# Kernel tuning notes

Measured on AMD Instinct MI355X. Metric: run time of the kernel, lower is better.

Reference implementation:

```python
import jax, jax.numpy as jnp
import numpy as np
from jax import lax

NUM_HEADS = 8
HEAD_DIM = 32  # filters_per_head


def conv1d_same(x, w, b):
    # x: [B, T, Cin], w: [K, Cin, Cout] (WIO), 'same' padding, stride 1
    y = lax.conv_general_dilated(x, w, window_strides=(1,), padding='SAME',
                                 dimension_numbers=('NWC', 'WIO', 'NWC'))
    return y + b


def setup_inputs() -> dict:
    key = jax.random.key(0)
    ks = jax.random.split(key, 9)
    B, T, C = 8, 2048, 256
    K = 3
    s = 1.0 / np.sqrt(K * C)
    return {
        'x': jax.random.normal(ks[0], (B, T, C), dtype=jnp.float32),
        'Wq': jax.random.normal(ks[1], (K, C, C), dtype=jnp.float32) * s,
        'bq': jnp.zeros((C,), dtype=jnp.float32),
        'Wk': jax.random.normal(ks[2], (K, C, C), dtype=jnp.float32) * s,
        'bk': jnp.zeros((C,), dtype=jnp.float32),
        'Wv': jax.random.normal(ks[3], (K, C, C), dtype=jnp.float32) * s,
        'bv': jnp.zeros((C,), dtype=jnp.float32),
        'Wo': jax.random.normal(ks[4], (K, C, C), dtype=jnp.float32) * s,
        'bo': jnp.zeros((C,), dtype=jnp.float32),
    }


def reference(x, Wq, bq, Wk, bk, Wv, bv, Wo, bo):
    B, T, C = x.shape
    q = conv1d_same(x, Wq, bq)
    k = conv1d_same(x, Wk, bk)
    v = conv1d_same(x, Wv, bv)

    def split(t):  # [B, T, C] -> [B, H, T, D]
        return t.reshape(B, T, NUM_HEADS, HEAD_DIM).transpose(0, 2, 1, 3)

    q, k, v = split(q), split(k), split(v)
    scale = 1.0 / jnp.sqrt(jnp.float32(HEAD_DIM))
    logits = jnp.einsum('bhqd,bhkd->bhqk', q, k) * scale  # [B,H,T,T]
    attn = jax.nn.softmax(logits, axis=-1)
    ctx = jnp.einsum('bhqk,bhkd->bhqd', attn, v)
    ctx = ctx.transpose(0, 2, 1, 3).reshape(B, T, C)
    out = x + conv1d_same(ctx, Wo, bo)
    return out
```

## Files before the change

### kernel.cpp

```cpp
#include <hip/hip_runtime.h>
#include <math.h>

#define BDIM 8
#define TDIM 2048
#define CDIM 256
#define HDIM 8
#define DDIM 32
#define TP   (TDIM + 2)

typedef __attribute__((ext_vector_type(8))) short bf16x8;
typedef __attribute__((ext_vector_type(4))) float f32x4;

#if __has_builtin(__builtin_amdgcn_exp2f)
#define EXP2(x) __builtin_amdgcn_exp2f(x)
#else
#define EXP2(x) exp2f(x)
#endif

__device__ __forceinline__ unsigned pk2(float lo, float hi) {
    union { float f; unsigned u; } a, b;
    a.f = lo; b.f = hi;
    return __builtin_amdgcn_perm(b.u + 0x8000u, a.u + 0x8000u, 0x07060302u);
}
__device__ __forceinline__ unsigned pk2t(float lo, float hi) {
    union { float f; unsigned u; } a, b;
    a.f = lo; b.f = hi;
    return __builtin_amdgcn_perm(b.u, a.u, 0x07060302u);
}
__device__ __forceinline__ short bf1(float v) {
    union { float f; unsigned u; } a; a.f = v;
    return (short)((a.u + 0x8000u) >> 16);
}
__device__ __forceinline__ void gld16(const short* g, short* l) {
    __builtin_amdgcn_global_load_lds((const __attribute__((address_space(1))) void*)g,
                                     (__attribute__((address_space(3))) void*)l, 16, 0, 0);
}

#define XBLK 832
#define WBLK 192

__global__ __launch_bounds__(256) void prep_kernel(
    const float* __restrict__ x,
    const float* __restrict__ Wq, const float* __restrict__ Wk,
    const float* __restrict__ Wv, const float* __restrict__ Wo,
    short* __restrict__ xbfp, short* __restrict__ cp,
    short* __restrict__ wcat, short* __restrict__ wot)
{
    const int tid = threadIdx.x;
    if (blockIdx.x < XBLK) {
        const int NX = BDIM * TDIM * 64;
        const int NH = 4096;
        unsigned* xw = (unsigned*)xbfp;
        unsigned* cw = (unsigned*)cp;
        for (int i = blockIdx.x * 256 + tid; i < NX + NH; i += XBLK * 256) {
            if (i < NX) {
                const int bt = i >> 6, c4 = i & 63;
                const int b = bt >> 11, t = bt & 2047;
                const float4 f = *(const float4*)(x + (size_t)bt * 256 + c4 * 4);
                const size_t wo_ = (size_t)(b * TP + t + 1) * 128 + c4 * 2;
                xw[wo_]     = pk2(f.x, f.y);
                xw[wo_ + 1] = pk2(f.z, f.w);
            } else {
                const int hz = i - NX;
                const int half = hz >> 11, z = hz & 2047;
                const int b = z >> 8, r = (z >> 7) & 1, wofs = z & 127;
                const size_t w_ = ((size_t)b * TP + (size_t)r * (TP - 1)) * 128 + wofs;
                if (half == 0) xw[w_] = 0u; else cw[w_] = 0u;
            }
        }
    } else {
        __shared__ float xs[64][65];
        const int wb = blockIdx.x - XBLK;
        const int pair = wb >> 4, sub = wb & 15;
        const int dt = pair >> 2, mat = pair & 3;
        const int ci0 = (sub >> 2) * 64, co0 = (sub & 3) * 64;
        const float* W = mat == 0 ? Wq : mat == 1 ? Wk : mat == 2 ? Wv : Wo;
        const float* src = W + dt * 65536 + (size_t)ci0 * 256 + co0;
        for (int idx = tid; idx < 4096; idx += 256) {
            const int r = idx >> 6, c = idx & 63;
            xs[r][c] = src[(size_t)r * 256 + c];
        }
        __syncthreads();
        short* dstbase = (mat < 3) ? (wcat + (size_t)(mat * 256 + co0) * 768)
                                   : (wot + (size_t)co0 * 768);
        for (int idx = tid; idx < 512; idx += 256) {
            const int co_l = idx >> 3, ci_l = (idx & 7) * 8;
            uint4 u;
            u.x = pk2(xs[ci_l + 0][co_l], xs[ci_l + 1][co_l]);
            u.y = pk2(xs[ci_l + 2][co_l], xs[ci_l + 3][co_l]);
            u.z = pk2(xs[ci_l + 4][co_l], xs[ci_l + 5][co_l]);
            u.w = pk2(xs[ci_l + 6][co_l], xs[ci_l + 7][co_l]);
            *(uint4*)(dstbase + (size_t)co_l * 768 + dt * 256 + ci0 + ci_l) = u;
        }
    }
}

__global__ __launch_bounds__(256) void gemm_qkv(
    const short* __restrict__ xbfp, const short* __restrict__ wcat,
    const float* __restrict__ bq, const float* __restrict__ bk,
    const float* __restrict__ bv,
    short* __restrict__ qo, short* __restrict__ ko, short* __restrict__ vt2)
{
    __shared__ short As[2][4096];
    __shared__ short Bs[2][4096];
    const int tid = threadIdx.x;
    const int wv = tid >> 6, lane = tid & 63, quad = lane >> 4, col = lane & 15;
    const int bx = blockIdx.x;
    const int b = bx >> 4, t0 = (bx & 15) * 128;
    const int by = blockIdx.y;
    const int qkv = by >> 1;
    const int m0 = by * 128;

    const short* wA = wcat + (size_t)m0 * 768;
    const short* xB = xbfp + ((size_t)b * TP + t0) * CDIM;
    const int r0 = tid >> 2, s0 = (tid & 3) * 8;

#define STAGE_Q(kk, bsel) do {                                                  \
    const int dt_ = (kk) >> 3, ci0_ = ((kk) & 7) * 32, k0_ = (kk) * 32;         \
    gld16(wA + (size_t)r0 * 768 + k0_ + s0,        &As[bsel][tid * 8]);         \
    gld16(wA + (size_t)(r0 + 64) * 768 + k0_ + s0, &As[bsel][tid * 8 + 2048]);  \
    gld16(xB + (size_t)(r0 + dt_) * 256 + ci0_ + s0,      &Bs[bsel][tid * 8]);  \
    gld16(xB + (size_t)(r0 + 64 + dt_) * 256 + ci0_ + s0, &Bs[bsel][tid * 8 + 2048]); \
} while (0)

    STAGE_Q(0, 0);

    const float* bias = qkv == 0 ? bq : qkv == 1 ? bk : bv;
    f32x4 acc[4][4];
#pragma unroll
    for (int mt = 0; mt < 4; ++mt) {
        const int cb = ((m0 + (wv & 1) * 64 + mt * 16) & 255) + quad * 4;
        const float4 b4 = *(const float4*)(bias + cb);
#pragma unroll
        for (int nt = 0; nt < 4; ++nt) acc[mt][nt] = (f32x4){b4.x, b4.y, b4.z, b4.w};
    }

    int bsel = 0;
    for (int kk = 0; kk < 24; ++kk) {
        __syncthreads();
        if (kk < 23) STAGE_Q(kk + 1, bsel ^ 1);
        const short* Ab = &As[bsel][((wv & 1) * 64 + col) * 32 + quad * 8];
        const short* Bb = &Bs[bsel][((wv >> 1) * 64 + col) * 32 + quad * 8];
        bf16x8 af[4], bfr[4];
#pragma unroll
        for (int i = 0; i < 4; ++i) {
            af[i]  = *(const bf16x8*)(Ab + i * 512);
            bfr[i] = *(const bf16x8*)(Bb + i * 512);
        }
#pragma unroll
        for (int mt = 0; mt < 4; ++mt)
#pragma unroll
            for (int nt = 0; nt < 4; ++nt)
                acc[mt][nt] = __builtin_amdgcn_mfma_f32_16x16x32_bf16(af[mt], bfr[nt], acc[mt][nt], 0, 0, 0);
        bsel ^= 1;
    }

    const float qs = 0.25503000508221157f;
#pragma unroll
    for (int mt = 0; mt < 4; ++mt) {
        const int cocat = m0 + (wv & 1) * 64 + mt * 16 + quad * 4;
        const int co = cocat & 255;
        const int hh = co >> 5, d = co & 31;
        const size_t bh = (size_t)b * HDIM + hh;
#pragma unroll
        for (int nt = 0; nt < 4; ++nt) {
            const int t = t0 + (wv >> 1) * 64 + nt * 16 + col;
            const f32x4 a = acc[mt][nt];
            if (qkv == 0) {
                uint2 u = make_uint2(pk2(a[0] * qs, a[1] * qs), pk2(a[2] * qs, a[3] * qs));
                *(uint2*)(qo + (bh * TDIM + t) * DDIM + d) = u;
            } else if (qkv == 1) {
                uint2 u = make_uint2(pk2(a[0], a[1]), pk2(a[2], a[3]));
                *(uint2*)(ko + (bh * TDIM + t) * DDIM + d) = u;
            } else {
                const int kt = t >> 6, u6 = t & 63, kg = u6 >> 5, rr = u6 & 31;
                const int j = ((rr >> 4) << 2) | (rr & 3), qd = (rr >> 2) & 3;
                short* vb2 = vt2 + ((bh * 32 + kt) * 2 + kg) * 1024 + qd * 8 + j;
#pragma unroll
                for (int r = 0; r < 4; ++r) vb2[(d + r) * 32] = bf1(a[r]);
            }
        }
    }
#undef STAGE_Q
}

__global__ __launch_bounds__(256) void gemm_res(
    const short* __restrict__ cp, const short* __restrict__ wot,
    const float* __restrict__ bo, const float* __restrict__ x,
    float* __restrict__ out)
{
    __shared__ short As[2][4096];
    __shared__ short Bs[2][4096];
    const int tid = threadIdx.x;
    const int wv = tid >> 6, lane = tid & 63, quad = lane >> 4, col = lane & 15;
    const int bx = blockIdx.x;
    const int b = bx >> 4, t0 = (bx & 15) * 128;
    const int m0 = blockIdx.y * 128;

    const short* wA = wot + (size_t)m0 * 768;
    const short* cB = cp + ((size_t)b * TP + t0) * CDIM;
    const int r0 = tid >> 2, s0 = (tid & 3) * 8;

#define STAGE_R(kk, bsel) do {                                                  \
    const int dt_ = (kk) >> 3, ci0_ = ((kk) & 7) * 32, k0_ = (kk) * 32;         \
    gld16(wA + (size_t)r0 * 768 + k0_ + s0,        &As[bsel][tid * 8]);         \
    gld16(wA + (size_t)(r0 + 64) * 768 + k0_ + s0, &As[bsel][tid * 8 + 2048]);  \
    gld16(cB + (size_t)(r0 + dt_) * 256 + ci0_ + s0,      &Bs[bsel][tid * 8]);  \
    gld16(cB + (size_t)(r0 + 64 + dt_) * 256 + ci0_ + s0, &Bs[bsel][tid * 8 + 2048]); \
} while (0)

    STAGE_R(0, 0);

    f32x4 acc[4][4];
#pragma unroll
    for (int mt = 0; mt < 4; ++mt) {
        const int cb = m0 + (wv & 1) * 64 + mt * 16 + quad * 4;
        const float4 b4 = *(const float4*)(bo + cb);
#pragma unroll
        for (int nt = 0; nt < 4; ++nt) acc[mt][nt] = (f32x4){b4.x, b4.y, b4.z, b4.w};
    }

    int bsel = 0;
    for (int kk = 0; kk < 24; ++kk) {
        __syncthreads();
        if (kk < 23) STAGE_R(kk + 1, bsel ^ 1);
        const short* Ab = &As[bsel][((wv & 1) * 64 + col) * 32 + quad * 8];
        const short* Bb = &Bs[bsel][((wv >> 1) * 64 + col) * 32 + quad * 8];
        bf16x8 af[4], bfr[4];
#pragma unroll
        for (int i = 0; i < 4; ++i) {
            af[i]  = *(const bf16x8*)(Ab + i * 512);
            bfr[i] = *(const bf16x8*)(Bb + i * 512);
        }
#pragma unroll
        for (int mt = 0; mt < 4; ++mt)
#pragma unroll
            for (int nt = 0; nt < 4; ++nt)
                acc[mt][nt] = __builtin_amdgcn_mfma_f32_16x16x32_bf16(af[mt], bfr[nt], acc[mt][nt], 0, 0, 0);
        bsel ^= 1;
    }

#pragma unroll
    for (int mt = 0; mt < 4; ++mt) {
        const int co = m0 + (wv & 1) * 64 + mt * 16 + quad * 4;
#pragma unroll
        for (int nt = 0; nt < 4; ++nt) {
            const int t = t0 + (wv >> 1) * 64 + nt * 16 + col;
            const size_t o = ((size_t)b * TDIM + t) * CDIM + co;
            const float4 xv = *(const float4*)(x + o);
            const f32x4 a = acc[mt][nt];
            *(float4*)(out + o) = make_float4(a[0] + xv.x, a[1] + xv.y, a[2] + xv.z, a[3] + xv.w);
        }
    }
#undef STAGE_R
}

__global__ __launch_bounds__(256, 4) void attn_kernel(
    const short* __restrict__ q, const short* __restrict__ k,
    const short* __restrict__ vt2, short* __restrict__ cp)
{
    const int tid = threadIdx.x;
    const int wv = tid >> 6, lane = tid & 63, quad = lane >> 4, col = lane & 15;
    const int bh = blockIdx.x;
    const int q0 = blockIdx.y * 128 + wv * 32;

    const short* qb = q + (size_t)bh * TDIM * DDIM;
    const int fo = col * 32 + quad * 8;
    const short* kp = k   + (size_t)bh * TDIM * DDIM + fo;
    const short* vp = vt2 + (size_t)bh * TDIM * DDIM + fo;

    bf16x8 qf[2];
    qf[0] = *(const bf16x8*)(qb + (size_t)(q0 + col) * DDIM + quad * 8);
    qf[1] = *(const bf16x8*)(qb + (size_t)(q0 + 16 + col) * DDIM + quad * 8);

    f32x4 acc0[2] = {{0.f,0.f,0.f,0.f},{0.f,0.f,0.f,0.f}};
    f32x4 acc1[2] = {{0.f,0.f,0.f,0.f},{0.f,0.f,0.f,0.f}};
    f32x4 accl[2] = {{0.f,0.f,0.f,0.f},{0.f,0.f,0.f,0.f}};
    const f32x4 zero = {0.f, 0.f, 0.f, 0.f};
    const short one_bf = (short)0x3F80;
    const bf16x8 ones = {one_bf, one_bf, one_bf, one_bf, one_bf, one_bf, one_bf, one_bf};

    bf16x8 kc[4], vf[4];
#pragma unroll
    for (int g = 0; g < 4; ++g) {
        kc[g] = *(const bf16x8*)(kp + g * 512);
        vf[g] = *(const bf16x8*)(vp + g * 512);
    }

#pragma unroll 2
    for (int kt = 0; kt < TDIM / 64; ++kt) {
        const int ntile = (kt + 1) & (TDIM / 64 - 1);
        bf16x8 kn[4], vn[4];
#pragma unroll
        for (int g = 0; g < 4; ++g) {
            kn[g] = *(const bf16x8*)(kp + ntile * 2048 + g * 512);
            vn[g] = *(const bf16x8*)(vp + ntile * 2048 + g * 512);
        }
#pragma unroll
        for (int qi = 0; qi < 2; ++qi) {
            f32x4 s[4];
            __builtin_amdgcn_s_setprio(1);
#pragma unroll
            for (int g = 0; g < 4; ++g)
                s[g] = __builtin_amdgcn_mfma_f32_16x16x32_bf16(kc[g], qf[qi], zero, 0, 0, 0);
            __builtin_amdgcn_s_setprio(0);
            float p[16];
#pragma unroll
            for (int g = 0; g < 4; ++g)
#pragma unroll
                for (int r = 0; r < 4; ++r)
                    p[g * 4 + r] = EXP2(s[g][r]);
            union { unsigned u[4]; bf16x8 v; } P0, P1;
            P0.u[0] = pk2t(p[0], p[1]);   P0.u[1] = pk2t(p[2], p[3]);
            P0.u[2] = pk2t(p[4], p[5]);   P0.u[3] = pk2t(p[6], p[7]);
            P1.u[0] = pk2t(p[8], p[9]);   P1.u[1] = pk2t(p[10], p[11]);
            P1.u[2] = pk2t(p[12], p[13]); P1.u[3] = pk2t(p[14], p[15]);
            __builtin_amdgcn_s_setprio(1);
            acc0[qi] = __builtin_amdgcn_mfma_f32_16x16x32_bf16(vf[0], P0.v, acc0[qi], 0, 0, 0);
            acc1[qi] = __builtin_amdgcn_mfma_f32_16x16x32_bf16(vf[1], P0.v, acc1[qi], 0, 0, 0);
            accl[qi] = __builtin_amdgcn_mfma_f32_16x16x32_bf16(ones,  P0.v, accl[qi], 0, 0, 0);
            acc0[qi] = __builtin_amdgcn_mfma_f32_16x16x32_bf16(vf[2], P1.v, acc0[qi], 0, 0, 0);
            acc1[qi] = __builtin_amdgcn_mfma_f32_16x16x32_bf16(vf[3], P1.v, acc1[qi], 0, 0, 0);
            accl[qi] = __builtin_amdgcn_mfma_f32_16x16x32_bf16(ones,  P1.v, accl[qi], 0, 0, 0);
            __builtin_amdgcn_s_setprio(0);
        }
#pragma unroll
        for (int g = 0; g < 4; ++g) { kc[g] = kn[g]; vf[g] = vn[g]; }
    }

    const int b = bh >> 3, hh = bh & 7;
#pragma unroll
    for (int qi = 0; qi < 2; ++qi) {
        const float inv = 1.f / accl[qi][0];
        const int t = q0 + qi * 16 + col;
        short* crow = cp + ((size_t)b * TP + t + 1) * CDIM + hh * DDIM;
        uint2 u0 = make_uint2(pk2(acc0[qi][0] * inv, acc0[qi][1] * inv),
                              pk2(acc0[qi][2] * inv, acc0[qi][3] * inv));
        uint2 u1 = make_uint2(pk2(acc1[qi][0] * inv, acc1[qi][1] * inv),
                              pk2(acc1[qi][2] * inv, acc1[qi][3] * inv));
        *(uint2*)(crow + quad * 4)      = u0;
        *(uint2*)(crow + 16 + quad * 4) = u1;
    }
}

extern "C" void kernel_launch(void* const* d_in, const int* in_sizes, int n_in,
                              void* d_out, int out_size, void* d_ws, size_t ws_size,
                              hipStream_t stream) {
    const float* x  = (const float*)d_in[0];
    const float* Wq = (const float*)d_in[1];
    const float* bq = (const float*)d_in[2];
    const float* Wk = (const float*)d_in[3];
    const float* bk = (const float*)d_in[4];
    const float* Wv = (const float*)d_in[5];
    const float* bv = (const float*)d_in[6];
    const float* Wo = (const float*)d_in[7];
    const float* bo = (const float*)d_in[8];
    float* out = (float*)d_out;

    short* p = (short*)d_ws;
    short* xbfp = p; p += (size_t)BDIM * TP * CDIM;
    short* cpb  = p; p += (size_t)BDIM * TP * CDIM;
    short* qbuf = p; p += (size_t)BDIM * HDIM * TDIM * DDIM;
    short* kbuf = p; p += (size_t)BDIM * HDIM * TDIM * DDIM;
    short* vt2  = p; p += (size_t)BDIM * HDIM * TDIM * DDIM;
    short* wcat = p; p += 768 * 768;
    short* wot  = p; p += 256 * 768;

    prep_kernel<<<dim3(XBLK + WBLK), 256, 0, stream>>>(x, Wq, Wk, Wv, Wo, xbfp, cpb, wcat, wot);
    gemm_qkv<<<dim3(128, 6), 256, 0, stream>>>(xbfp, wcat, bq, bk, bv, qbuf, kbuf, vt2);
    attn_kernel<<<dim3(64, 16), 256, 0, stream>>>(qbuf, kbuf, vt2, cpb);
    gemm_res<<<dim3(128, 2), 256, 0, stream>>>(cpb, wot, bo, x, out);
}
```

Measured before the change: 202.1 us.

## Stage K/V tiles through double-buffered swizzled LDS in attention kernel

The attention kernel now loads each 128-key K and V tile cooperatively into double-buffered shared memory with async global-to-LDS copies and an XOR swizzle, instead of having every wave read K/V directly from global memory into registers. The four waves of a block share each tile, so redundant global/L2 traffic is cut and the next tile is prefetched while the current one is computed. The key tile per iteration doubles from 64 to 128, which raises register pressure (8 K and 8 V fragments, 32 probabilities) and adds a block-wide barrier per iteration.

```diff
diff --git a/kernel.cpp b/kernel.cpp
--- a/kernel.cpp
+++ b/kernel.cpp
@@ -259,15 +259,32 @@
     const short* __restrict__ q, const short* __restrict__ k,
     const short* __restrict__ vt2, short* __restrict__ cp)
 {
+    __shared__ short ks[2][4096];
+    __shared__ short vs[2][4096];
     const int tid = threadIdx.x;
     const int wv = tid >> 6, lane = tid & 63, quad = lane >> 4, col = lane & 15;
     const int bh = blockIdx.x;
     const int q0 = blockIdx.y * 128 + wv * 32;
 
     const short* qb = q + (size_t)bh * TDIM * DDIM;
-    const int fo = col * 32 + quad * 8;
-    const short* kp = k   + (size_t)bh * TDIM * DDIM + fo;
-    const short* vp = vt2 + (size_t)bh * TDIM * DDIM + fo;
+    const short* kb = k + (size_t)bh * TDIM * DDIM;
+    const short* vb = vt2 + (size_t)bh * TDIM * DDIM;
+
+    const int c1 = tid, c2 = tid + 256;
+    const int g1 = ((c1 & ~3) | ((c1 & 3) ^ ((c1 >> 3) & 3))) * 8;
+    const int g2 = ((c2 & ~3) | ((c2 & 3) ^ ((c2 >> 3) & 3))) * 8;
+    const int l1 = c1 * 8, l2 = c2 * 8;
+
+#define STAGE_A(kt, bsel) do {                                   \
+    const short* kt_k = kb + (kt) * 4096;                        \
+    const short* kt_v = vb + (kt) * 4096;                        \
+    gld16(kt_k + g1, &ks[bsel][l1]);                             \
+    gld16(kt_k + g2, &ks[bsel][l2]);                             \
+    gld16(kt_v + g1, &vs[bsel][l1]);                             \
+    gld16(kt_v + g2, &vs[bsel][l2]);                             \
+} while (0)
+
+    STAGE_A(0, 0);
 
     bf16x8 qf[2];
     qf[0] = *(const bf16x8*)(qb + (size_t)(q0 + col) * DDIM + quad * 8);
@@ -280,52 +297,52 @@
     const short one_bf = (short)0x3F80;
     const bf16x8 ones = {one_bf, one_bf, one_bf, one_bf, one_bf, one_bf, one_bf, one_bf};
 
-    bf16x8 kc[4], vf[4];
-#pragma unroll
-    for (int g = 0; g < 4; ++g) {
-        kc[g] = *(const bf16x8*)(kp + g * 512);
-        vf[g] = *(const bf16x8*)(vp + g * 512);
-    }
-
+    const int foff = col * 32 + ((quad ^ ((col >> 1) & 3)) << 3);
+    __syncthreads();
+
+    int bsel = 0;
 #pragma unroll 2
-    for (int kt = 0; kt < TDIM / 64; ++kt) {
-        const int ntile = (kt + 1) & (TDIM / 64 - 1);
-        bf16x8 kn[4], vn[4];
-#pragma unroll
-        for (int g = 0; g < 4; ++g) {
-            kn[g] = *(const bf16x8*)(kp + ntile * 2048 + g * 512);
-            vn[g] = *(const bf16x8*)(vp + ntile * 2048 + g * 512);
+    for (int kt = 0; kt < TDIM / 128; ++kt) {
+        if (kt < TDIM / 128 - 1) STAGE_A(kt + 1, bsel ^ 1);
+        bf16x8 kc[8], vf[8];
+#pragma unroll
+        for (int g = 0; g < 8; ++g) {
+            kc[g] = *(const bf16x8*)&ks[bsel][g * 512 + foff];
+            vf[g] = *(const bf16x8*)&vs[bsel][g * 512 + foff];
         }
 #pragma unroll
         for (int qi = 0; qi < 2; ++qi) {
-            f32x4 s[4];
+            f32x4 s[8];
             __builtin_amdgcn_s_setprio(1);
 #pragma unroll
-            for (int g = 0; g < 4; ++g)
+            for (int g = 0; g < 8; ++g)
                 s[g] = __builtin_amdgcn_mfma_f32_16x16x32_bf16(kc[g], qf[qi], zero, 0, 0, 0);
             __builtin_amdgcn_s_setprio(0);
-            float p[16];
-#pragma unroll
-            for (int g = 0; g < 4; ++g)
+            float p[32];
+#pragma unroll
+            for (int g = 0; g < 8; ++g)
 #pragma unroll
                 for (int r = 0; r < 4; ++r)
                     p[g * 4 + r] = EXP2(s[g][r]);
-            union { unsigned u[4]; bf16x8 v; } P0, P1;
-            P0.u[0] = pk2t(p[0], p[1]);   P0.u[1] = pk2t(p[2], p[3]);
-            P0.u[2] = pk2t(p[4], p[5]);   P0.u[3] = pk2t(p[6], p[7]);
-            P1.u[0] = pk2t(p[8], p[9]);   P1.u[1] = pk2t(p[10], p[11]);
-            P1.u[2] = pk2t(p[12], p[13]); P1.u[3] = pk2t(p[14], p[15]);
+            union { unsigned u[4]; bf16x8 v; } P[4];
+#pragma unroll
+            for (int j = 0; j < 4; ++j) {
+                P[j].u[0] = pk2t(p[j * 8 + 0], p[j * 8 + 1]);
+                P[j].u[1] = pk2t(p[j * 8 + 2], p[j * 8 + 3]);
+                P[j].u[2] = pk2t(p[j * 8 + 4], p[j * 8 + 5]);
+                P[j].u[3] = pk2t(p[j * 8 + 6], p[j * 8 + 7]);
+            }
             __builtin_amdgcn_s_setprio(1);
-            acc0[qi] = __builtin_amdgcn_mfma_f32_16x16x32_bf16(vf[0], P0.v, acc0[qi], 0, 0, 0);
-            acc1[qi] = __builtin_amdgcn_mfma_f32_16x16x32_bf16(vf[1], P0.v, acc1[qi], 0, 0, 0);
-            accl[qi] = __builtin_amdgcn_mfma_f32_16x16x32_bf16(ones,  P0.v, accl[qi], 0, 0, 0);
-            acc0[qi] = __builtin_amdgcn_mfma_f32_16x16x32_bf16(vf[2], P1.v, acc0[qi], 0, 0, 0);
-            acc1[qi] = __builtin_amdgcn_mfma_f32_16x16x32_bf16(vf[3], P1.v, acc1[qi], 0, 0, 0);
-            accl[qi] = __builtin_amdgcn_mfma_f32_16x16x32_bf16(ones,  P1.v, accl[qi], 0, 0, 0);
+#pragma unroll
+            for (int j = 0; j < 4; ++j) {
+                acc0[qi] = __builtin_amdgcn_mfma_f32_16x16x32_bf16(vf[2 * j],     P[j].v, acc0[qi], 0, 0, 0);
+                acc1[qi] = __builtin_amdgcn_mfma_f32_16x16x32_bf16(vf[2 * j + 1], P[j].v, acc1[qi], 0, 0, 0);
+                accl[qi] = __builtin_amdgcn_mfma_f32_16x16x32_bf16(ones,          P[j].v, accl[qi], 0, 0, 0);
+            }
             __builtin_amdgcn_s_setprio(0);
         }
-#pragma unroll
-        for (int g = 0; g < 4; ++g) { kc[g] = kn[g]; vf[g] = vn[g]; }
+        __syncthreads();
+        bsel ^= 1;
     }
 
     const int b = bh >> 3, hh = bh & 7;
@@ -341,6 +358,7 @@
         *(uint2*)(crow + quad * 4)      = u0;
         *(uint2*)(crow + 16 + quad * 4) = u1;
     }
+#undef STAGE_A
 }
 
 extern "C" void kernel_launch(void* const* d_in, const int* in_sizes, int n_in,
```

After: 268.4 us. 1.33x slower.
